# Kernel tuning notes

Hardware: AMD Instinct MI355X
Metric: run time of the kernel (lower is better)

## Reference

```python
import jax, jax.numpy as jnp
import numpy as np

# dims: batch, seq, d_model, mlp_width, num_experts, lora_rank
B, S, D, M, E, R = 4, 1024, 2048, 5632, 8, 16
LORA_ALPHA = 32
SCALING = LORA_ALPHA / R  # = 2.0


def setup_inputs() -> dict:
    key = jax.random.key(0)
    ks = jax.random.split(key, 13)
    s = 0.02
    f32 = jnp.float32
    return {
        'x':  jax.random.normal(ks[0], (B, S, D), f32),
        # router: nn.Linear(d_model, num_experts)
        'Wr': jax.random.normal(ks[1], (E, D), f32) * s,
        'br': jax.random.normal(ks[2], (E,), f32) * s,
        # frozen original MLP weights (torch Linear layout [out, in])
        'Wg': jax.random.normal(ks[3], (M, D), f32) * s,
        'Wu': jax.random.normal(ks[4], (M, D), f32) * s,
        'Wd': jax.random.normal(ks[5], (D, M), f32) * s,
        # shared LoRA A matrices [rank, fan_in]
        'Ag': jax.random.normal(ks[6], (R, D), f32) * s,
        'Au': jax.random.normal(ks[7], (R, D), f32) * s,
        'Ad': jax.random.normal(ks[8], (R, M), f32) * s,
        # per-expert LoRA B matrices [E, fan_out, rank] (zero-init in the
        # original; randomized here so gradients/outputs are non-trivial)
        'Bg': jax.random.normal(ks[9], (E, M, R), f32) * s,
        'Bu': jax.random.normal(ks[10], (E, M, R), f32) * s,
        'Bd': jax.random.normal(ks[11], (E, D, R), f32) * s,
    }


def _lora_moe_dense(x, W, A, Bexp, routing):
    """Dense MoE LoRA: original_proj(x) + sum_e routing[...,e] * (x @ A^T @ B_e^T) * scaling.
    x: [b,s,in], W: [out,in], A: [r,in], Bexp: [E,out,r], routing: [b,s,E].
    Identical math to stacking all experts then weighted-summing, but the
    shared A lets us weight the tiny [b,s,E,r] hidden instead of [b,s,E,out].
    """
    orig = jnp.einsum('bsi,oi->bso', x, W)
    h = jnp.einsum('bsi,ri->bsr', x, A)            # shared low-rank hidden
    hw = jnp.einsum('bsr,bse->bser', h, routing)   # routing-weighted hidden
    lora = jnp.einsum('bser,eor->bso', hw, Bexp) * SCALING
    return orig + lora


def reference(x, Wr, br, Wg, Wu, Wd, Ag, Au, Ad, Bg, Bu, Bd):
    logits = jnp.einsum('bsd,ed->bse', x, Wr) + br
    routing = jax.nn.softmax(logits, axis=-1)
    idx = jnp.argmax(routing, axis=-1)
    y_hard = jax.nn.one_hot(idx, E, dtype=logits.dtype)
    # straight-through expert choice
    expert_choice = y_hard - jax.lax.stop_gradient(routing) + routing
    gate = _lora_moe_dense(x, Wg, Ag, Bg, routing)
    up = _lora_moe_dense(x, Wu, Au, Bu, routing)
    h = jax.nn.silu(gate) * up  # LLaMA-style SwiGLU act_fn
    out = _lora_moe_dense(h, Wd, Ad, Bd, routing)
    return out, routing, expert_choice
```

## Files before the change

kernel.cpp:

```cpp
#include <hip/hip_runtime.h>

#define DEV __device__ __forceinline__

typedef unsigned short u16;
typedef __bf16 bf16x8 __attribute__((ext_vector_type(8)));
typedef float f32x4 __attribute__((ext_vector_type(4)));

static DEV u16 f2bf(float f) {
    union { float f; unsigned u; } v; v.f = f;
    unsigned r = v.u + 0x7fffu + ((v.u >> 16) & 1u);
    return (u16)(r >> 16);
}
static DEV float bf2f(u16 u) {
    union { unsigned u; float f; } v; v.u = ((unsigned)u) << 16;
    return v.f;
}
static DEV void g2l16(const u16* g, u16* l) {
    __builtin_amdgcn_global_load_lds(
        (const __attribute__((address_space(1))) void*)g,
        (__attribute__((address_space(3))) void*)l, 16, 0, 0);
}

#define BAR()    do { __builtin_amdgcn_s_barrier(); __builtin_amdgcn_sched_barrier(0); } while (0)
#define WAITV(N) asm volatile("s_waitcnt vmcnt(" #N ")" ::: "memory")

#define MM16(A, B, FMO, FNO) do {                                            \
    __builtin_amdgcn_s_setprio(1);                                           \
    _Pragma("unroll")                                                        \
    for (int fm_ = 0; fm_ < 4; ++fm_)                                        \
      _Pragma("unroll")                                                      \
      for (int fn_ = 0; fn_ < 2; ++fn_)                                      \
        _Pragma("unroll")                                                    \
        for (int ks_ = 0; ks_ < 2; ++ks_)                                    \
          acc[(FMO) + fm_][(FNO) + fn_] = __builtin_amdgcn_mfma_f32_16x16x32_bf16( \
              A[fm_][ks_], B[fn_][ks_], acc[(FMO) + fm_][(FNO) + fn_], 0, 0, 0); \
    __builtin_amdgcn_s_setprio(0);                                           \
} while (0)


__global__ __launch_bounds__(256) void k_conv(
    const float* __restrict__ Wg, const float* __restrict__ Wu, const float* __restrict__ Wd,
    const float* __restrict__ Bg, const float* __restrict__ Bu, const float* __restrict__ Bd,
    u16* __restrict__ Wg16, u16* __restrict__ Wu16, u16* __restrict__ Wd16,
    u16* __restrict__ Bgx, u16* __restrict__ Bux, u16* __restrict__ Bdx)
{
    const long long NW = 2883584;
    const long long NB = 180224;
    const long long ND = 65536;
    long long gid = (long long)blockIdx.x * 256 + threadIdx.x;
    if (gid < 3 * NW) {
        const float* s; u16* d; long long g = gid;
        if (g < NW)           { s = Wg; d = Wg16; }
        else if (g < 2 * NW)  { s = Wu; d = Wu16; g -= NW; }
        else                  { s = Wd; d = Wd16; g -= 2 * NW; }
        float4 v = *(const float4*)(s + g * 4);
        ushort4 o; o.x = f2bf(v.x); o.y = f2bf(v.y); o.z = f2bf(v.z); o.w = f2bf(v.w);
        *(ushort4*)(d + g * 4) = o;
    } else {
        long long g = gid - 3 * NW;
        const float* s; u16* d; int nr;
        if (g < NB)               { s = Bg; d = Bgx; nr = 5632; }
        else if (g < 2 * NB)      { s = Bu; d = Bux; nr = 5632; g -= NB; }
        else if (g < 2 * NB + ND) { s = Bd; d = Bdx; nr = 2048; g -= 2 * NB; }
        else return;
        int n = (int)(g >> 5);
        int j0 = ((int)g & 31) * 4;
        int e = j0 >> 4, r0 = j0 & 15;
        float4 v = *(const float4*)&s[((size_t)e * nr + n) * 16 + r0];
        ushort4 o; o.x = f2bf(v.x); o.y = f2bf(v.y); o.z = f2bf(v.z); o.w = f2bf(v.w);
        *(ushort4*)&d[(size_t)n * 128 + j0] = o;
    }
}

__global__ __launch_bounds__(256) void k_router(
    const float* __restrict__ x, const float* __restrict__ Wr,
    const float* __restrict__ Ag, const float* __restrict__ Au,
    u16* __restrict__ x16, float* __restrict__ fin1)
{
    __shared__ float xs[64][65];
    __shared__ float wsm[40][64];
    const int rb = blockIdx.x, ksp = blockIdx.y;
    const int row0 = rb * 64;
    const int t = threadIdx.x;
    const int rloc = t & 63, og = t >> 6;
    float acc[10];
#pragma unroll
    for (int o = 0; o < 10; ++o) acc[o] = 0.f;

    for (int c4 = 0; c4 < 4; ++c4) {
        const int k0 = ksp * 256 + c4 * 64;
        __syncthreads();
#pragma unroll
        for (int i = 0; i < 4; ++i) {
            int idx = t + i * 256;
            int r = idx >> 4, c = (idx & 15) * 4;
            float4 v = *(const float4*)&x[(size_t)(row0 + r) * 2048 + k0 + c];
            xs[r][c + 0] = v.x; xs[r][c + 1] = v.y; xs[r][c + 2] = v.z; xs[r][c + 3] = v.w;
            ushort4 o; o.x = f2bf(v.x); o.y = f2bf(v.y); o.z = f2bf(v.z); o.w = f2bf(v.w);
            *(ushort4*)&x16[(size_t)(row0 + r) * 2048 + k0 + c] = o;
        }
#pragma unroll
        for (int i = 0; i < 3; ++i) {
            int idx = t + i * 256;
            if (idx < 640) {
                int r = idx >> 4, c = (idx & 15) * 4;
                const float* src = (r < 8) ? (Wr + (size_t)r * 2048)
                                : (r < 24) ? (Ag + (size_t)(r - 8) * 2048)
                                           : (Au + (size_t)(r - 24) * 2048);
                float4 v = *(const float4*)&src[k0 + c];
                wsm[r][c + 0] = v.x; wsm[r][c + 1] = v.y; wsm[r][c + 2] = v.z; wsm[r][c + 3] = v.w;
            }
        }
        __syncthreads();
#pragma unroll
        for (int k = 0; k < 64; ++k) {
            float xv = xs[rloc][k];
#pragma unroll
            for (int o = 0; o < 10; ++o) acc[o] += xv * wsm[og * 10 + o][k];
        }
    }
    float* dst = fin1 + ((size_t)ksp * 4096 + row0 + rloc) * 40 + og * 10;
#pragma unroll
    for (int o = 0; o < 10; ++o) dst[o] = acc[o];
}

__global__ __launch_bounds__(256) void k_fin1(
    const float* __restrict__ fin1, const float* __restrict__ br,
    float* __restrict__ routing_ws, float* __restrict__ out_rt, float* __restrict__ out_ec,
    u16* __restrict__ hwg, u16* __restrict__ hwu)
{
    const int row = blockIdx.x * 256 + threadIdx.x;
    float s[40];
#pragma unroll
    for (int j = 0; j < 40; ++j) s[j] = 0.f;
    for (int p = 0; p < 8; ++p) {
        const float* src = fin1 + ((size_t)p * 4096 + row) * 40;
#pragma unroll
        for (int j = 0; j < 40; ++j) s[j] += src[j];
    }
    float lg[8]; float m = -1e30f;
#pragma unroll
    for (int e = 0; e < 8; ++e) { lg[e] = s[e] + br[e]; m = fmaxf(m, lg[e]); }
    float ex[8]; float sum = 0.f;
#pragma unroll
    for (int e = 0; e < 8; ++e) { ex[e] = expf(lg[e] - m); sum += ex[e]; }
    float r8[8];
#pragma unroll
    for (int e = 0; e < 8; ++e) r8[e] = ex[e] / sum;
    int best = 0;
#pragma unroll
    for (int e = 1; e < 8; ++e) if (r8[e] > r8[best]) best = e;
#pragma unroll
    for (int e = 0; e < 8; ++e) {
        routing_ws[(size_t)row * 8 + e] = r8[e];
        out_rt[(size_t)row * 8 + e] = r8[e];
        float yh = (e == best) ? 1.f : 0.f;
        out_ec[(size_t)row * 8 + e] = (yh - r8[e]) + r8[e];
    }
#pragma unroll
    for (int e = 0; e < 8; ++e) {
        float re = r8[e];
#pragma unroll
        for (int rk = 0; rk < 16; ++rk) {
            hwg[(size_t)row * 128 + e * 16 + rk] = f2bf(2.f * s[8 + rk] * re);
            hwu[(size_t)row * 128 + e * 16 + rk] = f2bf(2.f * s[24 + rk] * re);
        }
    }
}

template<int MODE>
__global__ __launch_bounds__(512, 2) void k_gemm8(
    const u16* __restrict__ A0, int lda0,
    const u16* __restrict__ A1g, const u16* __restrict__ A1u,
    const u16* __restrict__ B0g, int ldb0, const u16* __restrict__ B0u,
    const u16* __restrict__ B1g, const u16* __restrict__ B1u,
    int Ksplit,
    float* __restrict__ outF0, float* __restrict__ outF1,
    u16* __restrict__ outHg, u16* __restrict__ outHu,
    int nbm, int nbn)
{
    __shared__ u16 lds[65536];
    const int t = threadIdx.x;
    const int nwg = (int)gridDim.x;
    const int orig = (int)blockIdx.x;
    const int sw = (orig & 7) * (nwg >> 3) + (orig >> 3);
    const int bm = sw % nbm; const int rest = sw / nbm;
    const int bn = rest % nbn; const int z = rest / nbn;

    const int row0 = bm * 256, col0 = bn * 256;
    int ktb, ntl;
    if (MODE == 0) { ktb = z ? 46 : 0; ntl = z ? 44 : 46; }
    else           { ktb = 0;          ntl = 34; }
    const int kend = ktb + ntl;
    const u16* A1 = (MODE == 1 && z) ? A1u : A1g;
    const u16* B0 = (MODE == 1 && z) ? B0u : B0g;
    const u16* B1 = (MODE == 1 && z) ? B1u : B1g;

    const int lane = t & 63, lr = lane & 15, lg = lane >> 4;
    const int wid = t >> 6, wr = wid >> 2, wcol = wid & 3;
    const int arow = wr * 128 + lr;
    const int brow = wcol * 64 + lr;
    const int sa = (arow & 7) << 3;
    const int sb = (brow & 7) << 3;

    const int rA = t >> 3;
    const int c00u = ((t & 7) * 8) ^ ((rA & 7) << 3);
    const u16* bA0 = A0 + (size_t)(row0 + rA) * lda0 + c00u;
    const u16* bA1 = A1 + ((size_t)(row0 + rA) << 7) + c00u;
    const u16* bB0 = B0 + (size_t)(col0 + rA) * ldb0 + c00u;
    const u16* bB1 = B1 + ((size_t)(col0 + rA) << 7) + c00u;
    const int ldsT = t * 8;

    auto stgA = [&](int kt, int h, int bufu) {
        const int k0 = kt * 64;
        const bool p2 = (k0 >= Ksplit);
        const u16* b = p2 ? (bA1 + (k0 - Ksplit)) : (bA0 + k0);
        const size_t ld = p2 ? (size_t)128 : (size_t)lda0;
        g2l16(b + (size_t)(h * 128) * ld,      &lds[bufu + h * 8192 + ldsT]);
        g2l16(b + (size_t)(h * 128 + 64) * ld, &lds[bufu + h * 8192 + 4096 + ldsT]);
    };
    auto stgB = [&](int kt, int h, int bufu) {
        const int k0 = kt * 64;
        const bool p2 = (k0 >= Ksplit);
        const u16* b = p2 ? (bB1 + (k0 - Ksplit)) : (bB0 + k0);
        const size_t ld = p2 ? (size_t)128 : (size_t)ldb0;
        g2l16(b + (size_t)(h * 128) * ld,      &lds[32768 + bufu + h * 8192 + ldsT]);
        g2l16(b + (size_t)(h * 128 + 64) * ld, &lds[32768 + bufu + h * 8192 + 4096 + ldsT]);
    };
    auto rdA = [&](int buf, int fb, bf16x8 (&d)[4][2]) {
#pragma unroll
        for (int fm = 0; fm < 4; ++fm)
#pragma unroll
            for (int ks = 0; ks < 2; ++ks)
                d[fm][ks] = *(const bf16x8*)&lds[buf * 16384 + (arow + (fb + fm) * 16) * 64
                                                 + (((ks << 5) | (lg << 3)) ^ sa)];
    };
    auto rdB = [&](int buf, int fb, bf16x8 (&d)[2][2]) {
#pragma unroll
        for (int fn = 0; fn < 2; ++fn)
#pragma unroll
            for (int ks = 0; ks < 2; ++ks)
                d[fn][ks] = *(const bf16x8*)&lds[32768 + buf * 16384 + (brow + (fb + fn) * 16) * 64
                                                 + (((ks << 5) | (lg << 3)) ^ sb)];
    };

    f32x4 acc[8][4];
    const f32x4 zf = {0.f, 0.f, 0.f, 0.f};
#pragma unroll
    for (int i = 0; i < 8; ++i)
#pragma unroll
        for (int j = 0; j < 4; ++j) acc[i][j] = zf;

    stgA(ktb, 0, 0); stgA(ktb, 1, 0);
    stgB(ktb, 0, 0); stgB(ktb, 1, 0);
    stgB(ktb + 1, 0, 16384); stgB(ktb + 1, 1, 16384);
    WAITV(4);
    BAR();

    const int ni = ntl >> 1;
    for (int i = 0; i < ni; ++i) {
        const int kt0 = ktb + 2 * i, kt1 = kt0 + 1;
        const bool s2 = (kt0 + 2 < kend), s3 = (kt1 + 2 < kend);
        bf16x8 alo[4][2], ahi[4][2], b01[2][2], b23[2][2];
        rdA(0, 0, alo); rdB(0, 0, b01);
        stgA(kt1, 0, 16384);
        BAR(); MM16(alo, b01, 0, 0); BAR();
        rdB(0, 2, b23);
        stgA(kt1, 1, 16384);
        BAR(); MM16(alo, b23, 0, 2); BAR();
        rdA(0, 4, ahi);
        if (s2) stgB(kt0 + 2, 0, 0);
        BAR(); MM16(ahi, b01, 4, 0); BAR();
        if (s2) { stgB(kt0 + 2, 1, 0); WAITV(4); } else { WAITV(0); }
        BAR(); MM16(ahi, b23, 4, 2); BAR();
        rdA(1, 0, alo); rdB(1, 0, b01);
        if (s2) stgA(kt0 + 2, 0, 0);
        BAR(); MM16(alo, b01, 0, 0); BAR();
        rdB(1, 2, b23);
        if (s2) stgA(kt0 + 2, 1, 0);
        BAR(); MM16(alo, b23, 0, 2); BAR();
        rdA(1, 4, ahi);
        if (s3) stgB(kt1 + 2, 0, 16384);
        BAR(); MM16(ahi, b01, 4, 0); BAR();
        if (s3) { stgB(kt1 + 2, 1, 16384); WAITV(4); } else { WAITV(0); }
        BAR(); MM16(ahi, b23, 4, 2); BAR();
    }

#pragma unroll
    for (int fm = 0; fm < 8; ++fm) {
#pragma unroll
        for (int fn = 0; fn < 4; ++fn) {
            const int r = row0 + wr * 128 + fm * 16 + lg * 4;
            const int c = col0 + wcol * 64 + fn * 16 + lr;
            f32x4 v = acc[fm][fn];
            if constexpr (MODE == 0) {
                float* out = z ? outF1 : outF0;
#pragma unroll
                for (int j = 0; j < 4; ++j) out[(size_t)(r + j) * 2048 + c] = v[j];
            } else {
                u16* out = z ? outHu : outHg;
#pragma unroll
                for (int j = 0; j < 4; ++j) out[(size_t)(r + j) * 5632 + c] = f2bf(v[j]);
            }
        }
    }
}

__global__ __launch_bounds__(256) void k_hd(
    u16* __restrict__ g, const u16* __restrict__ u,
    const float* __restrict__ Ad, float* __restrict__ fin2)
{
    __shared__ float hs[64][65];
    __shared__ float as2[16][64];
    const int rb = blockIdx.x, ksp = blockIdx.y;
    const int row0 = rb * 64;
    const int t = threadIdx.x;
    const int rloc = t & 63, og = t >> 6;
    float acc[4] = {0.f, 0.f, 0.f, 0.f};
    for (int c4 = 0; c4 < 11; ++c4) {
        const int k0 = ksp * 704 + c4 * 64;
        __syncthreads();
#pragma unroll
        for (int i = 0; i < 4; ++i) {
            int idx = t + i * 256;
            int r = idx >> 4, cc = (idx & 15) * 4;
            size_t go = (size_t)(row0 + r) * 5632 + k0 + cc;
            ushort4 gv = *(const ushort4*)&g[go];
            ushort4 uv = *(const ushort4*)&u[go];
            float h0, h1, h2, h3;
            { float gg = bf2f(gv.x); h0 = gg / (1.f + __expf(-gg)) * bf2f(uv.x); }
            { float gg = bf2f(gv.y); h1 = gg / (1.f + __expf(-gg)) * bf2f(uv.y); }
            { float gg = bf2f(gv.z); h2 = gg / (1.f + __expf(-gg)) * bf2f(uv.z); }
            { float gg = bf2f(gv.w); h3 = gg / (1.f + __expf(-gg)) * bf2f(uv.w); }
            hs[r][cc + 0] = h0; hs[r][cc + 1] = h1; hs[r][cc + 2] = h2; hs[r][cc + 3] = h3;
            ushort4 hv; hv.x = f2bf(h0); hv.y = f2bf(h1); hv.z = f2bf(h2); hv.w = f2bf(h3);
            *(ushort4*)&g[go] = hv;
        }
        {
            int r = t >> 4, cc = (t & 15) * 4;
            float4 w = *(const float4*)&Ad[(size_t)r * 5632 + k0 + cc];
            as2[r][cc + 0] = w.x; as2[r][cc + 1] = w.y; as2[r][cc + 2] = w.z; as2[r][cc + 3] = w.w;
        }
        __syncthreads();
#pragma unroll
        for (int k = 0; k < 64; ++k) {
            float hv = hs[rloc][k];
#pragma unroll
            for (int o = 0; o < 4; ++o) acc[o] += hv * as2[og * 4 + o][k];
        }
    }
    float* dst = fin2 + ((size_t)ksp * 4096 + row0 + rloc) * 16 + og * 4;
#pragma unroll
    for (int o = 0; o < 4; ++o) dst[o] = acc[o];
}

__global__ __launch_bounds__(256) void k_fin2(
    const float* __restrict__ fin2, const float* __restrict__ routing_ws, u16* __restrict__ hwd)
{
    const int row = blockIdx.x * 256 + threadIdx.x;
    float hd[16];
#pragma unroll
    for (int j = 0; j < 16; ++j) hd[j] = 0.f;
    for (int p = 0; p < 8; ++p) {
        const float* src = fin2 + ((size_t)p * 4096 + row) * 16;
#pragma unroll
        for (int j = 0; j < 16; ++j) hd[j] += src[j];
    }
#pragma unroll
    for (int e = 0; e < 8; ++e) {
        float re = routing_ws[(size_t)row * 8 + e];
#pragma unroll
        for (int rk = 0; rk < 16; ++rk)
            hwd[(size_t)row * 128 + e * 16 + rk] = f2bf(2.f * hd[rk] * re);
    }
}

__global__ __launch_bounds__(256) void k_reduce(
    float* __restrict__ o, const float* __restrict__ p1)
{
    size_t i = ((size_t)blockIdx.x * 256 + threadIdx.x) * 4;
    float4 a = *(const float4*)&o[i];
    float4 b = *(const float4*)&p1[i];
    float4 r; r.x = a.x + b.x; r.y = a.y + b.y; r.z = a.z + b.z; r.w = a.w + b.w;
    *(float4*)&o[i] = r;
}

extern "C" void kernel_launch(void* const* d_in, const int* in_sizes, int n_in,
                              void* d_out, int out_size, void* d_ws, size_t ws_size,
                              hipStream_t stream)
{
    (void)in_sizes; (void)n_in; (void)out_size; (void)ws_size;
    const float* x  = (const float*)d_in[0];
    const float* Wr = (const float*)d_in[1];
    const float* br = (const float*)d_in[2];
    const float* Wg = (const float*)d_in[3];
    const float* Wu = (const float*)d_in[4];
    const float* Wd = (const float*)d_in[5];
    const float* Ag = (const float*)d_in[6];
    const float* Au = (const float*)d_in[7];
    const float* Ad = (const float*)d_in[8];
    const float* Bg = (const float*)d_in[9];
    const float* Bu = (const float*)d_in[10];
    const float* Bd = (const float*)d_in[11];

    float* outp   = (float*)d_out;
    float* out_rt = outp + 8388608;
    float* out_ec = out_rt + 32768;

    char* p = (char*)d_ws;
    auto carve = [&](size_t n) -> char* { char* r = p; p += (n + 255) & ~(size_t)255; return r; };
    u16*   x16        = (u16*)carve(16777216);
    u16*   hwg        = (u16*)carve(1048576);
    u16*   hwu        = (u16*)carve(1048576);
    u16*   hwd        = (u16*)carve(1048576);
    float* routing_ws = (float*)carve(131072);
    float* fin1       = (float*)carve(5242880);
    float* fin2       = (float*)carve(2097152);
    u16*   Wg16       = (u16*)carve(23068672);
    u16*   Wu16       = (u16*)carve(23068672);
    u16*   Wd16       = (u16*)carve(23068672);
    u16*   Bgx        = (u16*)carve(1441792);
    u16*   Bux        = (u16*)carve(1441792);
    u16*   Bdx        = (u16*)carve(524288);
    u16*   gbuf       = (u16*)carve(46137344);
    u16*   ubuf       = (u16*)carve(46137344);
    float* part1      = (float*)ubuf;

    k_conv<<<dim3(35456), dim3(256), 0, stream>>>(Wg, Wu, Wd, Bg, Bu, Bd,
                                                  Wg16, Wu16, Wd16, Bgx, Bux, Bdx);
    k_router<<<dim3(64, 8), dim3(256), 0, stream>>>(x, Wr, Ag, Au, x16, fin1);
    k_fin1<<<dim3(16), dim3(256), 0, stream>>>(fin1, br, routing_ws, out_rt, out_ec, hwg, hwu);
    k_gemm8<1><<<dim3(704), dim3(512), 0, stream>>>(
        x16, 2048, hwg, hwu, Wg16, 2048, Wu16, Bgx, Bux,
        2048, (float*)nullptr, (float*)nullptr, gbuf, ubuf, 16, 22);
    k_hd<<<dim3(64, 8), dim3(256), 0, stream>>>(gbuf, ubuf, Ad, fin2);
    k_fin2<<<dim3(16), dim3(256), 0, stream>>>(fin2, routing_ws, hwd);
    k_gemm8<0><<<dim3(256), dim3(512), 0, stream>>>(
        gbuf, 5632, hwd, hwd, Wd16, 5632, Wd16, Bdx, Bdx,
        5632, outp, part1, (u16*)nullptr, (u16*)nullptr, 16, 8);
    k_reduce<<<dim3(8192), dim3(256), 0, stream>>>(outp, part1);
}
```

Before: 452.3 us.

## Halve barriers in GEMM main loop and spread fin kernels over more blocks

```diff
diff --git a/kernel.cpp b/kernel.cpp
--- a/kernel.cpp
+++ b/kernel.cpp
@@ -124,12 +124,12 @@
     for (int o = 0; o < 10; ++o) dst[o] = acc[o];
 }
 
-__global__ __launch_bounds__(256) void k_fin1(
+__global__ __launch_bounds__(64) void k_fin1(
     const float* __restrict__ fin1, const float* __restrict__ br,
     float* __restrict__ routing_ws, float* __restrict__ out_rt, float* __restrict__ out_ec,
     u16* __restrict__ hwg, u16* __restrict__ hwu)
 {
-    const int row = blockIdx.x * 256 + threadIdx.x;
+    const int row = blockIdx.x * 64 + threadIdx.x;
     float s[40];
 #pragma unroll
     for (int j = 0; j < 40; ++j) s[j] = 0.f;
@@ -227,20 +227,20 @@
         g2l16(b + (size_t)(h * 128) * ld,      &lds[32768 + bufu + h * 8192 + ldsT]);
         g2l16(b + (size_t)(h * 128 + 64) * ld, &lds[32768 + bufu + h * 8192 + 4096 + ldsT]);
     };
-    auto rdA = [&](int buf, int fb, bf16x8 (&d)[4][2]) {
+    auto rdA = [&](int bufu, int fb, bf16x8 (&d)[4][2]) {
 #pragma unroll
         for (int fm = 0; fm < 4; ++fm)
 #pragma unroll
             for (int ks = 0; ks < 2; ++ks)
-                d[fm][ks] = *(const bf16x8*)&lds[buf * 16384 + (arow + (fb + fm) * 16) * 64
+                d[fm][ks] = *(const bf16x8*)&lds[bufu + (arow + (fb + fm) * 16) * 64
                                                  + (((ks << 5) | (lg << 3)) ^ sa)];
     };
-    auto rdB = [&](int buf, int fb, bf16x8 (&d)[2][2]) {
+    auto rdB = [&](int bufu, int fb, bf16x8 (&d)[2][2]) {
 #pragma unroll
         for (int fn = 0; fn < 2; ++fn)
 #pragma unroll
             for (int ks = 0; ks < 2; ++ks)
-                d[fn][ks] = *(const bf16x8*)&lds[32768 + buf * 16384 + (brow + (fb + fn) * 16) * 64
+                d[fn][ks] = *(const bf16x8*)&lds[32768 + bufu + (brow + (fb + fn) * 16) * 64
                                                  + (((ks << 5) | (lg << 3)) ^ sb)];
     };
 
@@ -262,28 +262,28 @@
         const int kt0 = ktb + 2 * i, kt1 = kt0 + 1;
         const bool s2 = (kt0 + 2 < kend), s3 = (kt1 + 2 < kend);
         bf16x8 alo[4][2], ahi[4][2], b01[2][2], b23[2][2];
-        rdA(0, 0, alo); rdB(0, 0, b01);
-        stgA(kt1, 0, 16384);
-        BAR(); MM16(alo, b01, 0, 0); BAR();
-        rdB(0, 2, b23);
-        stgA(kt1, 1, 16384);
-        BAR(); MM16(alo, b23, 0, 2); BAR();
+        rdA(0, 0, alo); rdB(0, 0, b01); rdB(0, 2, b23);
+        stgA(kt1, 0, 16384); stgA(kt1, 1, 16384);
+        BAR();
+        MM16(alo, b01, 0, 0); MM16(alo, b23, 0, 2);
+        BAR();
         rdA(0, 4, ahi);
-        if (s2) stgB(kt0 + 2, 0, 0);
-        BAR(); MM16(ahi, b01, 4, 0); BAR();
-        if (s2) { stgB(kt0 + 2, 1, 0); WAITV(4); } else { WAITV(0); }
-        BAR(); MM16(ahi, b23, 4, 2); BAR();
-        rdA(1, 0, alo); rdB(1, 0, b01);
-        if (s2) stgA(kt0 + 2, 0, 0);
-        BAR(); MM16(alo, b01, 0, 0); BAR();
-        rdB(1, 2, b23);
-        if (s2) stgA(kt0 + 2, 1, 0);
-        BAR(); MM16(alo, b23, 0, 2); BAR();
-        rdA(1, 4, ahi);
-        if (s3) stgB(kt1 + 2, 0, 16384);
-        BAR(); MM16(ahi, b01, 4, 0); BAR();
-        if (s3) { stgB(kt1 + 2, 1, 16384); WAITV(4); } else { WAITV(0); }
-        BAR(); MM16(ahi, b23, 4, 2); BAR();
+        if (s2) { stgB(kt0 + 2, 0, 0); stgB(kt0 + 2, 1, 0); }
+        BAR();
+        MM16(ahi, b01, 4, 0); MM16(ahi, b23, 4, 2);
+        if (s2) { WAITV(4); } else { WAITV(0); }
+        BAR();
+        rdA(16384, 0, alo); rdB(16384, 0, b01); rdB(16384, 2, b23);
+        if (s2) { stgA(kt0 + 2, 0, 0); stgA(kt0 + 2, 1, 0); }
+        BAR();
+        MM16(alo, b01, 0, 0); MM16(alo, b23, 0, 2);
+        BAR();
+        rdA(16384, 4, ahi);
+        if (s3) { stgB(kt1 + 2, 0, 16384); stgB(kt1 + 2, 1, 16384); }
+        BAR();
+        MM16(ahi, b01, 4, 0); MM16(ahi, b23, 4, 2);
+        if (s3) { WAITV(4); }
+        BAR();
     }
 
 #pragma unroll
@@ -354,10 +354,10 @@
     for (int o = 0; o < 4; ++o) dst[o] = acc[o];
 }
 
-__global__ __launch_bounds__(256) void k_fin2(
+__global__ __launch_bounds__(64) void k_fin2(
     const float* __restrict__ fin2, const float* __restrict__ routing_ws, u16* __restrict__ hwd)
 {
-    const int row = blockIdx.x * 256 + threadIdx.x;
+    const int row = blockIdx.x * 64 + threadIdx.x;
     float hd[16];
 #pragma unroll
     for (int j = 0; j < 16; ++j) hd[j] = 0.f;
@@ -429,12 +429,12 @@
     k_conv<<<dim3(35456), dim3(256), 0, stream>>>(Wg, Wu, Wd, Bg, Bu, Bd,
                                                   Wg16, Wu16, Wd16, Bgx, Bux, Bdx);
     k_router<<<dim3(64, 8), dim3(256), 0, stream>>>(x, Wr, Ag, Au, x16, fin1);
-    k_fin1<<<dim3(16), dim3(256), 0, stream>>>(fin1, br, routing_ws, out_rt, out_ec, hwg, hwu);
+    k_fin1<<<dim3(64), dim3(64), 0, stream>>>(fin1, br, routing_ws, out_rt, out_ec, hwg, hwu);
     k_gemm8<1><<<dim3(704), dim3(512), 0, stream>>>(
         x16, 2048, hwg, hwu, Wg16, 2048, Wu16, Bgx, Bux,
         2048, (float*)nullptr, (float*)nullptr, gbuf, ubuf, 16, 22);
     k_hd<<<dim3(64, 8), dim3(256), 0, stream>>>(gbuf, ubuf, Ad, fin2);
-    k_fin2<<<dim3(16), dim3(256), 0, stream>>>(fin2, routing_ws, hwd);
+    k_fin2<<<dim3(64), dim3(64), 0, stream>>>(fin2, routing_ws, hwd);
     k_gemm8<0><<<dim3(256), dim3(512), 0, stream>>>(
         gbuf, 5632, hwd, hwd, Wd16, 5632, Wd16, Bdx, Bdx,
         5632, outp, part1, (u16*)nullptr, (u16*)nullptr, 16, 8);
```

After: 438.4 us. -3.1%, faster.
